# Kernel optimization log

Measured on AMD Instinct MI355X. Metric: run time of the kernel, lower is better.

Reference implementation:

```python
import jax, jax.numpy as jnp
import numpy as np

B, T, D = 16, 1024, 384
T_OUT = 4096  # fixed expanded length (mean duration 4 frames/token)


def setup_inputs() -> dict:
    key = jax.random.key(0)
    k_x, k_ids, k_noise = jax.random.split(key, 3)
    x = jax.random.normal(k_x, (B, T, D), dtype=jnp.float32)
    # Build integer durations that sum to exactly T_OUT per row by counting
    # T_OUT sorted segment assignments into T buckets.
    ids = jnp.sort(jax.random.randint(k_ids, (B, T_OUT), 0, T), axis=1)
    counts = jax.vmap(lambda r: jnp.zeros((T,), jnp.float32).at[r].add(1.0))(ids)
    # Add noise in (-0.4, 0.4) so floor(dur + 0.5) recovers counts but the
    # rounding path in the module is exercised with non-integer inputs.
    noise = jax.random.uniform(k_noise, (B, T), minval=-0.4, maxval=0.4)
    dur = counts + noise
    return {"x": x, "dur": dur, "out_len": T_OUT}


def reference(x, dur, out_len):
    # dur[dur < 0] = 0
    dur = jnp.maximum(dur, 0.0)
    # (dur + 0.5).long() -> truncation == floor for non-negative values
    counts = jnp.floor(dur + 0.5).astype(jnp.int32)  # [B, T]
    # repeat_interleave as a gather: output position j maps to the token i
    # whose cumulative-count interval contains j.
    csum = jnp.cumsum(counts, axis=1)                 # [B, T]
    pos = jnp.arange(out_len, dtype=jnp.int32)        # [T_out]
    idx = jax.vmap(lambda c: jnp.searchsorted(c, pos, side="right"))(csum)  # [B, T_out]
    idx = jnp.clip(idx, 0, x.shape[1] - 1)
    out = jnp.take_along_axis(x, idx[:, :, None], axis=1)  # [B, T_out, D]
    return out
```

## Files before the change

### kernel.cpp

```cpp
#include <hip/hip_runtime.h>
#include <hip/hip_bf16.h>


#define LR_B     16
#define LR_T     1024
#define LR_D4    96
#define LR_TOUT  4096

__global__ __launch_bounds__(LR_T) void lr_scan(
    const float* __restrict__ dur, int* __restrict__ csum) {
    const int b    = blockIdx.x;
    const int t    = threadIdx.x;
    const int lane = t & 63;
    const int wid  = t >> 6;

    float d = fmaxf(dur[b * LR_T + t], 0.0f);
    int v = (int)floorf(d + 0.5f);

    #pragma unroll
    for (int off = 1; off < 64; off <<= 1) {
        int u = __shfl_up(v, off, 64);
        if (lane >= off) v += u;
    }

    __shared__ int wsum[16];
    if (lane == 63) wsum[wid] = v;
    __syncthreads();

    if (wid == 0 && lane < 16) {
        int w = wsum[lane];
        #pragma unroll
        for (int off = 1; off < 16; off <<= 1) {
            int u = __shfl_up(w, off, 64);
            if (lane >= off) w += u;
        }
        wsum[lane] = w;
    }
    __syncthreads();

    const int offset = (wid == 0) ? 0 : wsum[wid - 1];
    csum[b * LR_T + t] = v + offset;
}

__global__ __launch_bounds__(384) void lr_write(
    const float4* __restrict__ x, const int* __restrict__ csum,
    float4* __restrict__ out) {
    const int blk = blockIdx.x;
    const int b   = blk >> 10;
    const int t   = blk & (LR_T - 1);
    const int tid = threadIdx.x;
    const int g   = tid / LR_D4;
    const int d   = tid - g * LR_D4;

    const int* cs = csum + b * LR_T;
    int end   = min(cs[t], LR_TOUT);
    int start = (t == 0) ? 0 : min(cs[t - 1], LR_TOUT);
    if (t == LR_T - 1) end = LR_TOUT;
    if (start >= end) return;

    const float4 v = x[(b * LR_T + t) * LR_D4 + d];
    float4* orow = out + (size_t)b * LR_TOUT * LR_D4 + d;
    for (int p = start + g; p < end; p += 4)
        orow[p * LR_D4] = v;
}

extern "C" void kernel_launch(void* const* d_in, const int* in_sizes, int n_in,
                              void* d_out, int out_size, void* d_ws, size_t ws_size,
                              hipStream_t stream) {
    const float* x   = (const float*)d_in[0];
    const float* dur = (const float*)d_in[1];

    int* csum = (int*)d_ws;

    lr_scan<<<LR_B, LR_T, 0, stream>>>(dur, csum);
    lr_write<<<LR_B * LR_T, 384, 0, stream>>>(
        (const float4*)x, csum, (float4*)d_out);
}
```

Before: 28.89 us.

## Fuse duration scan into expansion kernel via per-block prefix reduction

```diff
diff --git a/kernel.cpp b/kernel.cpp
--- a/kernel.cpp
+++ b/kernel.cpp
@@ -6,62 +6,50 @@
 #define LR_T     1024
 #define LR_D4    96
 #define LR_TOUT  4096
+#define LR_NTHR  384
 
-__global__ __launch_bounds__(LR_T) void lr_scan(
-    const float* __restrict__ dur, int* __restrict__ csum) {
-    const int b    = blockIdx.x;
-    const int t    = threadIdx.x;
-    const int lane = t & 63;
-    const int wid  = t >> 6;
-
-    float d = fmaxf(dur[b * LR_T + t], 0.0f);
-    int v = (int)floorf(d + 0.5f);
-
-    #pragma unroll
-    for (int off = 1; off < 64; off <<= 1) {
-        int u = __shfl_up(v, off, 64);
-        if (lane >= off) v += u;
-    }
-
-    __shared__ int wsum[16];
-    if (lane == 63) wsum[wid] = v;
-    __syncthreads();
-
-    if (wid == 0 && lane < 16) {
-        int w = wsum[lane];
-        #pragma unroll
-        for (int off = 1; off < 16; off <<= 1) {
-            int u = __shfl_up(w, off, 64);
-            if (lane >= off) w += u;
-        }
-        wsum[lane] = w;
-    }
-    __syncthreads();
-
-    const int offset = (wid == 0) ? 0 : wsum[wid - 1];
-    csum[b * LR_T + t] = v + offset;
+__device__ __forceinline__ int lr_count(float d) {
+    return (int)floorf(fmaxf(d, 0.0f) + 0.5f);
 }
 
-__global__ __launch_bounds__(384) void lr_write(
-    const float4* __restrict__ x, const int* __restrict__ csum,
+__global__ __launch_bounds__(LR_NTHR) void lr_fused(
+    const float* __restrict__ dur, const float4* __restrict__ x,
     float4* __restrict__ out) {
     const int blk = blockIdx.x;
     const int b   = blk >> 10;
     const int t   = blk & (LR_T - 1);
     const int tid = threadIdx.x;
-    const int g   = tid / LR_D4;
-    const int d   = tid - g * LR_D4;
 
-    const int* cs = csum + b * LR_T;
-    int end   = min(cs[t], LR_TOUT);
-    int start = (t == 0) ? 0 : min(cs[t - 1], LR_TOUT);
-    if (t == LR_T - 1) end = LR_TOUT;
+    const int g = tid / LR_D4;
+    const int d = tid - g * LR_D4;
+    const float4 v = x[(size_t)(b * LR_T + t) * LR_D4 + d];
+
+    const float* drow = dur + b * LR_T;
+    int sum = 0;
+    #pragma unroll
+    for (int k = 0; k < 3; ++k) {
+        int j = tid + k * LR_NTHR;
+        if (j <= t) sum += lr_count(drow[j]);
+    }
+    #pragma unroll
+    for (int off = 1; off < 64; off <<= 1)
+        sum += __shfl_xor(sum, off, 64);
+
+    __shared__ int wsum[LR_NTHR / 64];
+    if ((tid & 63) == 0) wsum[tid >> 6] = sum;
+    __syncthreads();
+    int end = wsum[0];
+    #pragma unroll
+    for (int w = 1; w < LR_NTHR / 64; ++w) end += wsum[w];
+
+    const int c = lr_count(drow[t]);
+    int start = min(end - c, LR_TOUT);
+    end = (t == LR_T - 1) ? LR_TOUT : min(end, LR_TOUT);
     if (start >= end) return;
 
-    const float4 v = x[(b * LR_T + t) * LR_D4 + d];
     float4* orow = out + (size_t)b * LR_TOUT * LR_D4 + d;
     for (int p = start + g; p < end; p += 4)
-        orow[p * LR_D4] = v;
+        orow[(size_t)p * LR_D4] = v;
 }
 
 extern "C" void kernel_launch(void* const* d_in, const int* in_sizes, int n_in,
@@ -70,9 +58,6 @@
     const float* x   = (const float*)d_in[0];
     const float* dur = (const float*)d_in[1];
 
-    int* csum = (int*)d_ws;
-
-    lr_scan<<<LR_B, LR_T, 0, stream>>>(dur, csum);
-    lr_write<<<LR_B * LR_T, 384, 0, stream>>>(
-        (const float4*)x, csum, (float4*)d_out);
+    lr_fused<<<LR_B * LR_T, LR_NTHR, 0, stream>>>(
+        dur, (const float4*)d_in[0], (float4*)d_out);
 }
```

New measurement: 30.16 us. +4.4%, slower.
